# Kernel tuning notes

Measured on AMD Instinct MI355X. Metric: run time of the kernel, lower is better.

## Reference

```python
import jax, jax.numpy as jnp
import numpy as np

N_NODES = 100000


def setup_inputs() -> dict:
    key = jax.random.key(0)
    k1, k2, k3, k4, k5, k6 = jax.random.split(key, 6)
    x = jax.random.normal(k1, (N_NODES, 256), dtype=jnp.float32)
    edge_index = jax.random.randint(k2, (2, 3200000), 0, N_NODES, dtype=jnp.int64)
    # GCNConv(256, 3): glorot weight + zero bias (PyG default)
    lim1 = float(np.sqrt(6.0 / (256 + 3)))
    W1 = jax.random.uniform(k3, (256, 3), minval=-lim1, maxval=lim1, dtype=jnp.float32)
    b1 = jnp.zeros((3,), dtype=jnp.float32)
    # Linear(3, 7): torch default kaiming-uniform-ish bounds
    lim2 = float(1.0 / np.sqrt(3))
    W2 = jax.random.uniform(k4, (3, 7), minval=-lim2, maxval=lim2, dtype=jnp.float32)
    b2 = jax.random.uniform(k5, (7,), minval=-lim2, maxval=lim2, dtype=jnp.float32)
    return {"x": x, "edge_index": edge_index, "W1": W1, "b1": b1, "W2": W2, "b2": b2}


def gcn_conv(x, edge_index, W, b, num_nodes):
    # PyG GCNConv: add self-loops, symmetric deg^-1/2 (A+I) deg^-1/2 normalization,
    # aggregate transformed features, then add bias.
    loop = jnp.arange(num_nodes, dtype=edge_index.dtype)
    src = jnp.concatenate([edge_index[0], loop])
    dst = jnp.concatenate([edge_index[1], loop])
    ones = jnp.ones_like(dst, dtype=x.dtype)
    deg = jax.ops.segment_sum(ones, dst, num_segments=num_nodes)  # [N]
    dinv = jnp.where(deg > 0, jax.lax.rsqrt(deg), 0.0)
    norm = dinv[src] * dinv[dst]  # [E+N]
    h = x @ W  # [N, 3] — transform BEFORE gather (small width)
    msg = h[src] * norm[:, None]  # [E+N, 3]
    agg = jax.ops.segment_sum(msg, dst, num_segments=num_nodes)  # [N, 3]
    return agg + b


def reference(x, edge_index, W1, b1, W2, b2):
    h = jax.nn.relu(gcn_conv(x, edge_index, W1, b1, x.shape[0]))  # [N, 3]
    z = h @ W2 + b2  # [N, 7]
    return (h, z)
```

## Files before the change

kernel.cpp:

```cpp
#include <hip/hip_runtime.h>
#include <stdint.h>


#define BSHIFT 8
#define BNODES 256
#define OVFCAP 8192
#define STRIDE 64
#define PSTRIDE 192

__device__ __forceinline__ bool ei_is64(const unsigned* __restrict__ ei) {
    const int t = threadIdx.x;
    const int nz = (t < 256) && (ei[2 * t + 1] != 0u);
    return __syncthreads_or(nz) == 0;
}

__global__ __launch_bounds__(512) void k_pre(const float* __restrict__ x,
                                             const float* __restrict__ W1,
                                             float* __restrict__ g4,
                                             const unsigned* __restrict__ ei,
                                             unsigned* __restrict__ records,
                                             unsigned* __restrict__ pcnt,
                                             unsigned* __restrict__ ovf_cnt,
                                             unsigned* __restrict__ ovf,
                                             int E, int B, int CAP, int CH,
                                             int nbin, int N) {
    const bool is64 = ei_is64(ei);
    if ((int)blockIdx.x < nbin) {
        __shared__ unsigned cursor[512];
        for (int i = threadIdx.x; i < B; i += 512) cursor[i] = 0u;
        __syncthreads();
        const int e0 = blockIdx.x * CH;
        const int e1 = min(E, e0 + CH);
        const unsigned sbase = blockIdx.x * STRIDE;

        auto emit = [&](unsigned s, unsigned d) {
            const unsigned bb  = d >> BSHIFT;
            const unsigned idx = atomicAdd(&cursor[bb], 1u);
            if (idx < STRIDE) {
                records[(size_t)bb * CAP + sbase + idx] = (s << BSHIFT) | (d & (BNODES - 1));
            } else {
                const unsigned o = atomicAdd(ovf_cnt, 1u);
                if (o < OVFCAP) { ovf[2 * o] = s; ovf[2 * o + 1] = d; }
            }
        };

        const int nq = (e1 - e0) >> 2;
        if (is64) {
            const unsigned long long* e64 = (const unsigned long long*)ei;
            const ulonglong2* sp = (const ulonglong2*)(e64 + e0);
            const ulonglong2* dp = (const ulonglong2*)(e64 + (size_t)E + e0);
            for (int q = threadIdx.x; q < nq; q += 512) {
                const ulonglong2 sa = sp[2 * q], sb = sp[2 * q + 1];
                const ulonglong2 da = dp[2 * q], db = dp[2 * q + 1];
                emit((unsigned)sa.x, (unsigned)da.x);
                emit((unsigned)sa.y, (unsigned)da.y);
                emit((unsigned)sb.x, (unsigned)db.x);
                emit((unsigned)sb.y, (unsigned)db.y);
            }
            for (int e = e0 + 4 * nq + threadIdx.x; e < e1; e += 512)
                emit((unsigned)e64[e], (unsigned)e64[(size_t)E + e]);
        } else {
            const uint4* sp = (const uint4*)(ei + e0);
            const uint4* dp = (const uint4*)(ei + (size_t)E + e0);
            for (int q = threadIdx.x; q < nq; q += 512) {
                const uint4 s4 = sp[q], d4 = dp[q];
                emit(s4.x, d4.x);
                emit(s4.y, d4.y);
                emit(s4.z, d4.z);
                emit(s4.w, d4.w);
            }
            for (int e = e0 + 4 * nq + threadIdx.x; e < e1; e += 512)
                emit(ei[e], ei[(size_t)E + e]);
        }
        __syncthreads();
        for (int i = threadIdx.x; i < B; i += 512)
            pcnt[(size_t)i * PSTRIDE + blockIdx.x] = min(cursor[i], (unsigned)STRIDE);
    } else {
        const int bx      = blockIdx.x - nbin;
        const int gtid    = bx * 512 + threadIdx.x;
        const int nthread = ((int)gridDim.x - nbin) * 512;
        const int lane    = threadIdx.x & 63;
        float w[4][3];
#pragma unroll
        for (int k = 0; k < 4; ++k)
#pragma unroll
            for (int c = 0; c < 3; ++c)
                w[k][c] = W1[(lane * 4 + k) * 3 + c];
        const int wave   = gtid >> 6;
        const int nwaves = nthread >> 6;
        for (int node = wave; node < N; node += nwaves) {
            const float4 v = *reinterpret_cast<const float4*>(x + (size_t)node * 256 + lane * 4);
            float s0 = v.x * w[0][0] + v.y * w[1][0] + v.z * w[2][0] + v.w * w[3][0];
            float s1 = v.x * w[0][1] + v.y * w[1][1] + v.z * w[2][1] + v.w * w[3][1];
            float s2 = v.x * w[0][2] + v.y * w[1][2] + v.z * w[2][2] + v.w * w[3][2];
#pragma unroll
            for (int off = 32; off > 0; off >>= 1) {
                s0 += __shfl_xor(s0, off, 64);
                s1 += __shfl_xor(s1, off, 64);
                s2 += __shfl_xor(s2, off, 64);
            }
            if (lane == 0)
                reinterpret_cast<float4*>(g4)[node] = make_float4(s0, s1, s2, 0.f);
        }
    }
}

__global__ __launch_bounds__(256) void k_cnt2(const unsigned* __restrict__ records,
                                              const unsigned* __restrict__ pcnt,
                                              const unsigned* __restrict__ ovf_cnt,
                                              const unsigned* __restrict__ ovf,
                                              unsigned* __restrict__ pcount,
                                              int B, int CAP, int SPLIT, int nbin) {
    __shared__ unsigned cnt[BNODES];
    __shared__ unsigned scnt[PSTRIDE];
    const int b  = blockIdx.x / SPLIT;
    const int sl = blockIdx.x - b * SPLIT;
    cnt[threadIdx.x] = 0u;
    for (int i = threadIdx.x; i < nbin; i += 256) scnt[i] = pcnt[(size_t)b * PSTRIDE + i];
    __syncthreads();
    const int per = CAP / SPLIT;
    const int lo = sl * per, hi = lo + per;
    const unsigned* rec = records + (size_t)b * CAP;
    for (int k = lo + threadIdx.x; k < hi; k += 256) {
        if ((unsigned)(k & (STRIDE - 1)) < scnt[k >> 6])
            atomicAdd(&cnt[rec[k] & (BNODES - 1)], 1u);
    }
    if (sl == 0) {
        unsigned no = *ovf_cnt; if (no > OVFCAP) no = OVFCAP;
        for (unsigned i = threadIdx.x; i < no; i += 256) {
            const unsigned d = ovf[2 * i + 1];
            if ((int)(d >> BSHIFT) == b) atomicAdd(&cnt[d & (BNODES - 1)], 1u);
        }
    }
    __syncthreads();
    pcount[((size_t)blockIdx.x << BSHIFT) + threadIdx.x] = cnt[threadIdx.x];
}

__global__ __launch_bounds__(256) void k_dinv2(const unsigned* __restrict__ pcount,
                                               float* __restrict__ g4, int N, int SPLIT) {
    const int i = blockIdx.x * 256 + threadIdx.x;
    if (i >= N) return;
    const int b = i >> BSHIFT, t = i & (BNODES - 1);
    unsigned deg = 1u;
    for (int s = 0; s < SPLIT; ++s)
        deg += pcount[(((size_t)b * SPLIT + s) << BSHIFT) + t];
    const float r = rsqrtf((float)deg);
    const float4 h = reinterpret_cast<const float4*>(g4)[i];
    reinterpret_cast<float4*>(g4)[i] = make_float4(h.x * r, h.y * r, h.z * r, r);
}

__global__ __launch_bounds__(256) void k_msg2(const unsigned* __restrict__ records,
                                              const unsigned* __restrict__ pcnt,
                                              const unsigned* __restrict__ ovf_cnt,
                                              const unsigned* __restrict__ ovf,
                                              const float* __restrict__ g4,
                                              float* __restrict__ psum,
                                              int B, int CAP, int SPLIT, int nbin) {
    __shared__ float acc[BNODES * 3];
    __shared__ unsigned scnt[PSTRIDE];
    const int b  = blockIdx.x / SPLIT;
    const int sl = blockIdx.x - b * SPLIT;
    for (int i = threadIdx.x; i < BNODES * 3; i += 256) acc[i] = 0.f;
    for (int i = threadIdx.x; i < nbin; i += 256) scnt[i] = pcnt[(size_t)b * PSTRIDE + i];
    __syncthreads();
    const int per = CAP / SPLIT;
    const int lo = sl * per, hi = lo + per;
    const unsigned* rec = records + (size_t)b * CAP;
    const float4* g4v = reinterpret_cast<const float4*>(g4);
    for (int k = lo + threadIdx.x; k < hi; k += 256) {
        if ((unsigned)(k & (STRIDE - 1)) < scnt[k >> 6]) {
            const unsigned r = rec[k];
            const float4 g = g4v[r >> BSHIFT];
            const unsigned l = (r & (BNODES - 1)) * 3;
            atomicAdd(&acc[l + 0], g.x);
            atomicAdd(&acc[l + 1], g.y);
            atomicAdd(&acc[l + 2], g.z);
        }
    }
    if (sl == 0) {
        unsigned no = *ovf_cnt; if (no > OVFCAP) no = OVFCAP;
        for (unsigned i = threadIdx.x; i < no; i += 256) {
            const unsigned d = ovf[2 * i + 1];
            if ((int)(d >> BSHIFT) == b) {
                const float4 g = g4v[ovf[2 * i]];
                const unsigned l = (d & (BNODES - 1)) * 3;
                atomicAdd(&acc[l + 0], g.x);
                atomicAdd(&acc[l + 1], g.y);
                atomicAdd(&acc[l + 2], g.z);
            }
        }
    }
    __syncthreads();
    const size_t base = ((size_t)blockIdx.x * 3) << BSHIFT;
    psum[base +   0 + threadIdx.x] = acc[threadIdx.x * 3 + 0];
    psum[base + 256 + threadIdx.x] = acc[threadIdx.x * 3 + 1];
    psum[base + 512 + threadIdx.x] = acc[threadIdx.x * 3 + 2];
}

__global__ __launch_bounds__(256) void k_fin(const float* __restrict__ psum,
                                             const float* __restrict__ g4,
                                             const float* __restrict__ b1,
                                             const float* __restrict__ W2,
                                             const float* __restrict__ b2,
                                             float* __restrict__ out, int N, int SPLIT) {
    const int i = blockIdx.x * 256 + threadIdx.x;
    if (i >= N) return;
    const int b = i >> BSHIFT, t = i & (BNODES - 1);
    float a0 = 0.f, a1 = 0.f, a2 = 0.f;
    for (int s = 0; s < SPLIT; ++s) {
        const size_t base = (((size_t)b * SPLIT + s) * 3) << BSHIFT;
        a0 += psum[base + t];
        a1 += psum[base + 256 + t];
        a2 += psum[base + 512 + t];
    }
    const float4 g = reinterpret_cast<const float4*>(g4)[i];
    const float  r = g.w;
    const float h0 = fmaxf(r * (a0 + g.x) + b1[0], 0.f);
    const float h1 = fmaxf(r * (a1 + g.y) + b1[1], 0.f);
    const float h2 = fmaxf(r * (a2 + g.z) + b1[2], 0.f);
    out[3 * (size_t)i + 0] = h0;
    out[3 * (size_t)i + 1] = h1;
    out[3 * (size_t)i + 2] = h2;
    float* z = out + (size_t)3 * N;
#pragma unroll
    for (int c = 0; c < 7; ++c)
        z[7 * (size_t)i + c] = h0 * W2[c] + h1 * W2[7 + c] + h2 * W2[14 + c] + b2[c];
}

__global__ __launch_bounds__(256) void k_xw1_fb(const float* __restrict__ x,
                                                const float* __restrict__ W1,
                                                float* __restrict__ g4,
                                                unsigned* __restrict__ zptr,
                                                int nzero, int N) {
    const int gtid = blockIdx.x * 256 + threadIdx.x;
    const int nthread = gridDim.x * 256;
    for (int i = gtid; i < nzero; i += nthread) zptr[i] = 0u;
    const int lane = threadIdx.x & 63;
    float w[4][3];
#pragma unroll
    for (int k = 0; k < 4; ++k)
#pragma unroll
        for (int c = 0; c < 3; ++c) w[k][c] = W1[(lane * 4 + k) * 3 + c];
    const int wave = gtid >> 6, nwaves = nthread >> 6;
    for (int node = wave; node < N; node += nwaves) {
        const float4 v = *reinterpret_cast<const float4*>(x + (size_t)node * 256 + lane * 4);
        float s0 = v.x * w[0][0] + v.y * w[1][0] + v.z * w[2][0] + v.w * w[3][0];
        float s1 = v.x * w[0][1] + v.y * w[1][1] + v.z * w[2][1] + v.w * w[3][1];
        float s2 = v.x * w[0][2] + v.y * w[1][2] + v.z * w[2][2] + v.w * w[3][2];
#pragma unroll
        for (int off = 32; off > 0; off >>= 1) {
            s0 += __shfl_xor(s0, off, 64);
            s1 += __shfl_xor(s1, off, 64);
            s2 += __shfl_xor(s2, off, 64);
        }
        if (lane == 0)
            reinterpret_cast<float4*>(g4)[node] = make_float4(s0, s1, s2, 0.f);
    }
}
__global__ __launch_bounds__(256) void k_deg_fb(const unsigned* __restrict__ ei,
                                                float* __restrict__ deg, int E) {
    const bool is64 = ei_is64(ei);
    const int e = blockIdx.x * 256 + threadIdx.x;
    if (e >= E) return;
    const unsigned d = is64 ? (unsigned)((const unsigned long long*)ei)[(size_t)E + e]
                            : ei[(size_t)E + e];
    atomicAdd(&deg[d], 1.0f);
}
__global__ __launch_bounds__(256) void k_dinv_fb(const float* __restrict__ deg,
                                                 float* __restrict__ g4, int N) {
    const int i = blockIdx.x * 256 + threadIdx.x;
    if (i >= N) return;
    const float r = rsqrtf(1.0f + deg[i]);
    const float4 h = reinterpret_cast<const float4*>(g4)[i];
    reinterpret_cast<float4*>(g4)[i] = make_float4(h.x * r, h.y * r, h.z * r, r);
}
__global__ __launch_bounds__(256) void k_edge_fb(const unsigned* __restrict__ ei,
                                                 const float* __restrict__ g4,
                                                 float* __restrict__ u4, int E) {
    const bool is64 = ei_is64(ei);
    const int e = blockIdx.x * 256 + threadIdx.x;
    if (e >= E) return;
    unsigned s, d;
    if (is64) {
        const unsigned long long* q = (const unsigned long long*)ei;
        s = (unsigned)q[e]; d = (unsigned)q[(size_t)E + e];
    } else {
        s = ei[e]; d = ei[(size_t)E + e];
    }
    const float4 g = reinterpret_cast<const float4*>(g4)[s];
    atomicAdd(&u4[4 * (size_t)d + 0], g.x);
    atomicAdd(&u4[4 * (size_t)d + 1], g.y);
    atomicAdd(&u4[4 * (size_t)d + 2], g.z);
}
__global__ __launch_bounds__(256) void k_final_fb(const float* __restrict__ u4,
                                                  const float* __restrict__ g4,
                                                  const float* __restrict__ b1,
                                                  const float* __restrict__ W2,
                                                  const float* __restrict__ b2,
                                                  float* __restrict__ out, int N) {
    const int i = blockIdx.x * 256 + threadIdx.x;
    if (i >= N) return;
    const float4 g = reinterpret_cast<const float4*>(g4)[i];
    const float4 u = reinterpret_cast<const float4*>(u4)[i];
    const float  r = g.w;
    const float h0 = fmaxf(r * (u.x + g.x) + b1[0], 0.f);
    const float h1 = fmaxf(r * (u.y + g.y) + b1[1], 0.f);
    const float h2 = fmaxf(r * (u.z + g.z) + b1[2], 0.f);
    out[3 * (size_t)i + 0] = h0;
    out[3 * (size_t)i + 1] = h1;
    out[3 * (size_t)i + 2] = h2;
    float* z = out + (size_t)3 * N;
#pragma unroll
    for (int c = 0; c < 7; ++c)
        z[7 * (size_t)i + c] = h0 * W2[c] + h1 * W2[7 + c] + h2 * W2[14 + c] + b2[c];
}

extern "C" void kernel_launch(void* const* d_in, const int* in_sizes, int n_in,
                              void* d_out, int out_size, void* d_ws, size_t ws_size,
                              hipStream_t stream) {
    const float*    x   = (const float*)d_in[0];
    const unsigned* ei  = (const unsigned*)d_in[1];
    const float*    W1  = (const float*)d_in[2];
    const float*    b1  = (const float*)d_in[3];
    const float*    W2  = (const float*)d_in[4];
    const float*    b2  = (const float*)d_in[5];
    float*          out = (float*)d_out;

    const int N = in_sizes[0] / 256;
    const int E = in_sizes[1] / 2;
    const int B = (N + BNODES - 1) >> BSHIFT;

    int CH   = ((E + 189) / 190 + 3) & ~3;
    int nbin = (E + CH - 1) / CH;
    int CAP  = nbin * STRIDE;

    char*     ws      = (char*)d_ws;
    unsigned* ovf_cnt = (unsigned*)ws;
    size_t off = 256;
    float*    g4  = (float*)(ws + off);
    off = (off + 16ull * N + 255) & ~(size_t)255;
    unsigned* ovf = (unsigned*)(ws + off);
    off = (off + 8ull * OVFCAP + 255) & ~(size_t)255;
    unsigned* pcnt = (unsigned*)(ws + off);
    off = (off + 4ull * B * PSTRIDE + 255) & ~(size_t)255;
    const size_t puoff = off;

    int SPLIT = 0;
    size_t rec_off = 0;
    const int sps[4] = {8, 4, 2, 1};
    for (int si = 0; si < 4; ++si) {
        const int sp = sps[si];
        const size_t ro = (puoff + 4ull * B * sp * 768 + 255) & ~(size_t)255;
        if (ws_size >= ro + 4ull * B * CAP + 4096) { SPLIT = sp; rec_off = ro; break; }
    }

    if (SPLIT) {
        unsigned* pcount  = (unsigned*)(ws + puoff);
        float*    psum    = (float*)(ws + puoff);
        unsigned* records = (unsigned*)(ws + rec_off);
        hipMemsetAsync(ovf_cnt, 0, 4, stream);
        const int NBX = 2048;
        k_pre<<<nbin + NBX, 512, 0, stream>>>(x, W1, g4, ei, records, pcnt,
                                              ovf_cnt, ovf, E, B, CAP, CH, nbin, N);
        k_cnt2<<<B * SPLIT, 256, 0, stream>>>(records, pcnt, ovf_cnt, ovf, pcount,
                                              B, CAP, SPLIT, nbin);
        k_dinv2<<<(N + 255) / 256, 256, 0, stream>>>(pcount, g4, N, SPLIT);
        k_msg2<<<B * SPLIT, 256, 0, stream>>>(records, pcnt, ovf_cnt, ovf, g4, psum,
                                              B, CAP, SPLIT, nbin);
        k_fin<<<(N + 255) / 256, 256, 0, stream>>>(psum, g4, b1, W2, b2, out, N, SPLIT);
    } else {
        float* deg = (float*)(ws + puoff);
        float* u4  = deg + N;
        k_xw1_fb<<<4096, 256, 0, stream>>>(x, W1, g4, (unsigned*)deg, 5 * N, N);
        k_deg_fb<<<(E + 255) / 256, 256, 0, stream>>>(ei, deg, E);
        k_dinv_fb<<<(N + 255) / 256, 256, 0, stream>>>(deg, g4, N);
        k_edge_fb<<<(E + 255) / 256, 256, 0, stream>>>(ei, g4, u4, E);
        k_final_fb<<<(N + 255) / 256, 256, 0, stream>>>(u4, g4, b1, W2, b2, out, N);
    }
}
```

Before: 116.5 us.

## Use finer edge-binning geometry, higher split, and 4-nodes-per-wave GEMV

```diff
diff --git a/kernel.cpp b/kernel.cpp
--- a/kernel.cpp
+++ b/kernel.cpp
@@ -5,8 +5,7 @@
 #define BSHIFT 8
 #define BNODES 256
 #define OVFCAP 8192
-#define STRIDE 64
-#define PSTRIDE 192
+#define PSTRIDE 1024
 
 __device__ __forceinline__ bool ei_is64(const unsigned* __restrict__ ei) {
     const int t = threadIdx.x;
@@ -14,6 +13,7 @@
     return __syncthreads_or(nz) == 0;
 }
 
+template <int SSH>
 __global__ __launch_bounds__(512) void k_pre(const float* __restrict__ x,
                                              const float* __restrict__ W1,
                                              float* __restrict__ g4,
@@ -31,12 +31,12 @@
         __syncthreads();
         const int e0 = blockIdx.x * CH;
         const int e1 = min(E, e0 + CH);
-        const unsigned sbase = blockIdx.x * STRIDE;
+        const unsigned sbase = blockIdx.x << SSH;
 
         auto emit = [&](unsigned s, unsigned d) {
             const unsigned bb  = d >> BSHIFT;
             const unsigned idx = atomicAdd(&cursor[bb], 1u);
-            if (idx < STRIDE) {
+            if (idx < (1u << SSH)) {
                 records[(size_t)bb * CAP + sbase + idx] = (s << BSHIFT) | (d & (BNODES - 1));
             } else {
                 const unsigned o = atomicAdd(ovf_cnt, 1u);
@@ -74,37 +74,50 @@
         }
         __syncthreads();
         for (int i = threadIdx.x; i < B; i += 512)
-            pcnt[(size_t)i * PSTRIDE + blockIdx.x] = min(cursor[i], (unsigned)STRIDE);
+            pcnt[(size_t)i * PSTRIDE + blockIdx.x] = min(cursor[i], 1u << SSH);
     } else {
         const int bx      = blockIdx.x - nbin;
         const int gtid    = bx * 512 + threadIdx.x;
         const int nthread = ((int)gridDim.x - nbin) * 512;
         const int lane    = threadIdx.x & 63;
-        float w[4][3];
-#pragma unroll
-        for (int k = 0; k < 4; ++k)
-#pragma unroll
-            for (int c = 0; c < 3; ++c)
-                w[k][c] = W1[(lane * 4 + k) * 3 + c];
+        const int fg      = lane & 15;
+        const int m       = lane >> 4;
+        float w[4][4][3];
+#pragma unroll
+        for (int p = 0; p < 4; ++p)
+#pragma unroll
+            for (int j = 0; j < 4; ++j)
+#pragma unroll
+                for (int c = 0; c < 3; ++c)
+                    w[p][j][c] = W1[(fg * 4 + p * 64 + j) * 3 + c];
         const int wave   = gtid >> 6;
         const int nwaves = nthread >> 6;
-        for (int node = wave; node < N; node += nwaves) {
-            const float4 v = *reinterpret_cast<const float4*>(x + (size_t)node * 256 + lane * 4);
-            float s0 = v.x * w[0][0] + v.y * w[1][0] + v.z * w[2][0] + v.w * w[3][0];
-            float s1 = v.x * w[0][1] + v.y * w[1][1] + v.z * w[2][1] + v.w * w[3][1];
-            float s2 = v.x * w[0][2] + v.y * w[1][2] + v.z * w[2][2] + v.w * w[3][2];
-#pragma unroll
-            for (int off = 32; off > 0; off >>= 1) {
+        for (int nb4 = wave * 4; nb4 < N; nb4 += nwaves * 4) {
+            const int node = nb4 + m;
+            float s0 = 0.f, s1 = 0.f, s2 = 0.f;
+            if (node < N) {
+                const float* row = x + (size_t)node * 256 + fg * 4;
+#pragma unroll
+                for (int p = 0; p < 4; ++p) {
+                    const float4 v = *reinterpret_cast<const float4*>(row + p * 64);
+                    s0 += v.x * w[p][0][0] + v.y * w[p][1][0] + v.z * w[p][2][0] + v.w * w[p][3][0];
+                    s1 += v.x * w[p][0][1] + v.y * w[p][1][1] + v.z * w[p][2][1] + v.w * w[p][3][1];
+                    s2 += v.x * w[p][0][2] + v.y * w[p][1][2] + v.z * w[p][2][2] + v.w * w[p][3][2];
+                }
+            }
+#pragma unroll
+            for (int off = 8; off >= 1; off >>= 1) {
                 s0 += __shfl_xor(s0, off, 64);
                 s1 += __shfl_xor(s1, off, 64);
                 s2 += __shfl_xor(s2, off, 64);
             }
-            if (lane == 0)
+            if (fg == 0 && node < N)
                 reinterpret_cast<float4*>(g4)[node] = make_float4(s0, s1, s2, 0.f);
         }
     }
 }
 
+template <int SSH>
 __global__ __launch_bounds__(256) void k_cnt2(const unsigned* __restrict__ records,
                                               const unsigned* __restrict__ pcnt,
                                               const unsigned* __restrict__ ovf_cnt,
@@ -122,7 +135,7 @@
     const int lo = sl * per, hi = lo + per;
     const unsigned* rec = records + (size_t)b * CAP;
     for (int k = lo + threadIdx.x; k < hi; k += 256) {
-        if ((unsigned)(k & (STRIDE - 1)) < scnt[k >> 6])
+        if ((unsigned)(k & ((1 << SSH) - 1)) < scnt[k >> SSH])
             atomicAdd(&cnt[rec[k] & (BNODES - 1)], 1u);
     }
     if (sl == 0) {
@@ -149,6 +162,7 @@
     reinterpret_cast<float4*>(g4)[i] = make_float4(h.x * r, h.y * r, h.z * r, r);
 }
 
+template <int SSH>
 __global__ __launch_bounds__(256) void k_msg2(const unsigned* __restrict__ records,
                                               const unsigned* __restrict__ pcnt,
                                               const unsigned* __restrict__ ovf_cnt,
@@ -168,7 +182,7 @@
     const unsigned* rec = records + (size_t)b * CAP;
     const float4* g4v = reinterpret_cast<const float4*>(g4);
     for (int k = lo + threadIdx.x; k < hi; k += 256) {
-        if ((unsigned)(k & (STRIDE - 1)) < scnt[k >> 6]) {
+        if ((unsigned)(k & ((1 << SSH) - 1)) < scnt[k >> SSH]) {
             const unsigned r = rec[k];
             const float4 g = g4v[r >> BSHIFT];
             const unsigned l = (r & (BNODES - 1)) * 3;
@@ -330,9 +344,12 @@
     const int E = in_sizes[1] / 2;
     const int B = (N + BNODES - 1) >> BSHIFT;
 
-    int CH   = ((E + 189) / 190 + 3) & ~3;
-    int nbin = (E + CH - 1) / CH;
-    int CAP  = nbin * STRIDE;
+    const int CH_A   = ((E + 1019) / 1020 + 3) & ~3;
+    const int nbin_A = (E + CH_A - 1) / CH_A;
+    const int CAP_A  = nbin_A << 4;
+    const int CH_B   = ((E + 189) / 190 + 3) & ~3;
+    const int nbin_B = (E + CH_B - 1) / CH_B;
+    const int CAP_B  = nbin_B << 6;
 
     char*     ws      = (char*)d_ws;
     unsigned* ovf_cnt = (unsigned*)ws;
@@ -345,29 +362,55 @@
     off = (off + 4ull * B * PSTRIDE + 255) & ~(size_t)255;
     const size_t puoff = off;
 
-    int SPLIT = 0;
-    size_t rec_off = 0;
-    const int sps[4] = {8, 4, 2, 1};
-    for (int si = 0; si < 4; ++si) {
-        const int sp = sps[si];
-        const size_t ro = (puoff + 4ull * B * sp * 768 + 255) & ~(size_t)255;
-        if (ws_size >= ro + 4ull * B * CAP + 4096) { SPLIT = sp; rec_off = ro; break; }
-    }
-
-    if (SPLIT) {
+    struct Cfg { int ssh, nbin, cap, ch, split; size_t rec_off; };
+    Cfg cfg{0, 0, 0, 0, 0, 0};
+    const int geo_ssh[2]  = {4, 6};
+    const int geo_nbin[2] = {nbin_A, nbin_B};
+    const int geo_cap[2]  = {CAP_A, CAP_B};
+    const int geo_ch[2]   = {CH_A, CH_B};
+    const int sps[3]      = {16, 8, 4};
+    for (int gi = 0; gi < 2 && !cfg.split; ++gi) {
+        for (int si = 0; si < 3 && !cfg.split; ++si) {
+            const int sp = sps[si];
+            const size_t ro = (puoff + 4ull * B * sp * 768 + 255) & ~(size_t)255;
+            if (ws_size >= ro + 4ull * B * geo_cap[gi] + 4096) {
+                cfg.ssh = geo_ssh[gi]; cfg.nbin = geo_nbin[gi]; cfg.cap = geo_cap[gi];
+                cfg.ch = geo_ch[gi]; cfg.split = sp; cfg.rec_off = ro;
+            }
+        }
+    }
+
+    if (cfg.split) {
         unsigned* pcount  = (unsigned*)(ws + puoff);
         float*    psum    = (float*)(ws + puoff);
-        unsigned* records = (unsigned*)(ws + rec_off);
+        unsigned* records = (unsigned*)(ws + cfg.rec_off);
         hipMemsetAsync(ovf_cnt, 0, 4, stream);
-        const int NBX = 2048;
-        k_pre<<<nbin + NBX, 512, 0, stream>>>(x, W1, g4, ei, records, pcnt,
-                                              ovf_cnt, ovf, E, B, CAP, CH, nbin, N);
-        k_cnt2<<<B * SPLIT, 256, 0, stream>>>(records, pcnt, ovf_cnt, ovf, pcount,
-                                              B, CAP, SPLIT, nbin);
-        k_dinv2<<<(N + 255) / 256, 256, 0, stream>>>(pcount, g4, N, SPLIT);
-        k_msg2<<<B * SPLIT, 256, 0, stream>>>(records, pcnt, ovf_cnt, ovf, g4, psum,
-                                              B, CAP, SPLIT, nbin);
-        k_fin<<<(N + 255) / 256, 256, 0, stream>>>(psum, g4, b1, W2, b2, out, N, SPLIT);
+        const int NBX = 1024;
+        if (cfg.ssh == 4) {
+            k_pre<4><<<cfg.nbin + NBX, 512, 0, stream>>>(x, W1, g4, ei, records, pcnt,
+                                                         ovf_cnt, ovf, E, B, cfg.cap,
+                                                         cfg.ch, cfg.nbin, N);
+            k_cnt2<4><<<B * cfg.split, 256, 0, stream>>>(records, pcnt, ovf_cnt, ovf,
+                                                         pcount, B, cfg.cap, cfg.split,
+                                                         cfg.nbin);
+        } else {
+            k_pre<6><<<cfg.nbin + NBX, 512, 0, stream>>>(x, W1, g4, ei, records, pcnt,
+                                                         ovf_cnt, ovf, E, B, cfg.cap,
+                                                         cfg.ch, cfg.nbin, N);
+            k_cnt2<6><<<B * cfg.split, 256, 0, stream>>>(records, pcnt, ovf_cnt, ovf,
+                                                         pcount, B, cfg.cap, cfg.split,
+                                                         cfg.nbin);
+        }
+        k_dinv2<<<(N + 255) / 256, 256, 0, stream>>>(pcount, g4, N, cfg.split);
+        if (cfg.ssh == 4)
+            k_msg2<4><<<B * cfg.split, 256, 0, stream>>>(records, pcnt, ovf_cnt, ovf, g4,
+                                                         psum, B, cfg.cap, cfg.split,
+                                                         cfg.nbin);
+        else
+            k_msg2<6><<<B * cfg.split, 256, 0, stream>>>(records, pcnt, ovf_cnt, ovf, g4,
+                                                         psum, B, cfg.cap, cfg.split,
+                                                         cfg.nbin);
+        k_fin<<<(N + 255) / 256, 256, 0, stream>>>(psum, g4, b1, W2, b2, out, N, cfg.split);
     } else {
         float* deg = (float*)(ws + puoff);
         float* u4  = deg + N;
```

New measurement: 150.3 us. 29.0% more time.

## Split X·W1 and edge binning into separate kernels with finer strips

Applied to the files above, without the earlier changes.

```diff
diff --git a/kernel.cpp b/kernel.cpp
--- a/kernel.cpp
+++ b/kernel.cpp
@@ -4,9 +4,10 @@
 
 #define BSHIFT 8
 #define BNODES 256
-#define OVFCAP 8192
-#define STRIDE 64
-#define PSTRIDE 192
+#define OVFCAP 16384
+#define PSTRIDE 1024
+#define SSH 4
+#define SPLITC 4
 
 __device__ __forceinline__ bool ei_is64(const unsigned* __restrict__ ei) {
     const int t = threadIdx.x;
@@ -14,116 +15,138 @@
     return __syncthreads_or(nz) == 0;
 }
 
-__global__ __launch_bounds__(512) void k_pre(const float* __restrict__ x,
+__global__ __launch_bounds__(512) void k_xw1(const float* __restrict__ x,
                                              const float* __restrict__ W1,
-                                             float* __restrict__ g4,
-                                             const unsigned* __restrict__ ei,
-                                             unsigned* __restrict__ records,
-                                             unsigned* __restrict__ pcnt,
-                                             unsigned* __restrict__ ovf_cnt,
-                                             unsigned* __restrict__ ovf,
-                                             int E, int B, int CAP, int CH,
-                                             int nbin, int N) {
-    const bool is64 = ei_is64(ei);
-    if ((int)blockIdx.x < nbin) {
-        __shared__ unsigned cursor[512];
-        for (int i = threadIdx.x; i < B; i += 512) cursor[i] = 0u;
-        __syncthreads();
-        const int e0 = blockIdx.x * CH;
-        const int e1 = min(E, e0 + CH);
-        const unsigned sbase = blockIdx.x * STRIDE;
-
-        auto emit = [&](unsigned s, unsigned d) {
-            const unsigned bb  = d >> BSHIFT;
-            const unsigned idx = atomicAdd(&cursor[bb], 1u);
-            if (idx < STRIDE) {
-                records[(size_t)bb * CAP + sbase + idx] = (s << BSHIFT) | (d & (BNODES - 1));
-            } else {
-                const unsigned o = atomicAdd(ovf_cnt, 1u);
-                if (o < OVFCAP) { ovf[2 * o] = s; ovf[2 * o + 1] = d; }
-            }
-        };
-
-        const int nq = (e1 - e0) >> 2;
-        if (is64) {
-            const unsigned long long* e64 = (const unsigned long long*)ei;
-            const ulonglong2* sp = (const ulonglong2*)(e64 + e0);
-            const ulonglong2* dp = (const ulonglong2*)(e64 + (size_t)E + e0);
-            for (int q = threadIdx.x; q < nq; q += 512) {
-                const ulonglong2 sa = sp[2 * q], sb = sp[2 * q + 1];
-                const ulonglong2 da = dp[2 * q], db = dp[2 * q + 1];
-                emit((unsigned)sa.x, (unsigned)da.x);
-                emit((unsigned)sa.y, (unsigned)da.y);
-                emit((unsigned)sb.x, (unsigned)db.x);
-                emit((unsigned)sb.y, (unsigned)db.y);
-            }
-            for (int e = e0 + 4 * nq + threadIdx.x; e < e1; e += 512)
-                emit((unsigned)e64[e], (unsigned)e64[(size_t)E + e]);
-        } else {
-            const uint4* sp = (const uint4*)(ei + e0);
-            const uint4* dp = (const uint4*)(ei + (size_t)E + e0);
-            for (int q = threadIdx.x; q < nq; q += 512) {
-                const uint4 s4 = sp[q], d4 = dp[q];
-                emit(s4.x, d4.x);
-                emit(s4.y, d4.y);
-                emit(s4.z, d4.z);
-                emit(s4.w, d4.w);
-            }
-            for (int e = e0 + 4 * nq + threadIdx.x; e < e1; e += 512)
-                emit(ei[e], ei[(size_t)E + e]);
-        }
-        __syncthreads();
-        for (int i = threadIdx.x; i < B; i += 512)
-            pcnt[(size_t)i * PSTRIDE + blockIdx.x] = min(cursor[i], (unsigned)STRIDE);
-    } else {
-        const int bx      = blockIdx.x - nbin;
-        const int gtid    = bx * 512 + threadIdx.x;
-        const int nthread = ((int)gridDim.x - nbin) * 512;
-        const int lane    = threadIdx.x & 63;
-        float w[4][3];
-#pragma unroll
-        for (int k = 0; k < 4; ++k)
-#pragma unroll
-            for (int c = 0; c < 3; ++c)
-                w[k][c] = W1[(lane * 4 + k) * 3 + c];
-        const int wave   = gtid >> 6;
-        const int nwaves = nthread >> 6;
-        for (int node = wave; node < N; node += nwaves) {
-            const float4 v = *reinterpret_cast<const float4*>(x + (size_t)node * 256 + lane * 4);
-            float s0 = v.x * w[0][0] + v.y * w[1][0] + v.z * w[2][0] + v.w * w[3][0];
-            float s1 = v.x * w[0][1] + v.y * w[1][1] + v.z * w[2][1] + v.w * w[3][1];
-            float s2 = v.x * w[0][2] + v.y * w[1][2] + v.z * w[2][2] + v.w * w[3][2];
-#pragma unroll
-            for (int off = 32; off > 0; off >>= 1) {
+                                             float4* __restrict__ part4, int N) {
+    const int gtid   = blockIdx.x * 512 + threadIdx.x;
+    const int wave   = gtid >> 6;
+    const int nwaves = (gridDim.x * 512) >> 6;
+    const int lane   = threadIdx.x & 63;
+    const int fg     = lane & 15;
+    const int m      = lane >> 4;
+    const int f      = wave & 3;
+    const int wq     = wave >> 2;
+    const int wstep  = nwaves >> 2;
+
+    float w[4][3];
+#pragma unroll
+    for (int j = 0; j < 4; ++j)
+#pragma unroll
+        for (int c = 0; c < 3; ++c)
+            w[j][c] = W1[(f * 64 + fg * 4 + j) * 3 + c];
+
+    const int nq = (N + 3) >> 2;
+    for (int q = wq; q < nq; q += 4 * wstep) {
+        int nd[4]; bool ok[4]; float4 v[4];
+#pragma unroll
+        for (int u = 0; u < 4; ++u) {
+            const int qu = q + u * wstep;
+            nd[u] = qu * 4 + m;
+            ok[u] = (qu < nq) && (nd[u] < N);
+            v[u]  = ok[u] ? *reinterpret_cast<const float4*>(
+                                x + (size_t)nd[u] * 256 + f * 64 + fg * 4)
+                          : make_float4(0.f, 0.f, 0.f, 0.f);
+        }
+#pragma unroll
+        for (int u = 0; u < 4; ++u) {
+            float s0 = v[u].x * w[0][0] + v[u].y * w[1][0] + v[u].z * w[2][0] + v[u].w * w[3][0];
+            float s1 = v[u].x * w[0][1] + v[u].y * w[1][1] + v[u].z * w[2][1] + v[u].w * w[3][1];
+            float s2 = v[u].x * w[0][2] + v[u].y * w[1][2] + v[u].z * w[2][2] + v[u].w * w[3][2];
+#pragma unroll
+            for (int off = 8; off >= 1; off >>= 1) {
                 s0 += __shfl_xor(s0, off, 64);
                 s1 += __shfl_xor(s1, off, 64);
                 s2 += __shfl_xor(s2, off, 64);
             }
-            if (lane == 0)
-                reinterpret_cast<float4*>(g4)[node] = make_float4(s0, s1, s2, 0.f);
-        }
-    }
-}
-
-__global__ __launch_bounds__(256) void k_cnt2(const unsigned* __restrict__ records,
+            if (ok[u] && fg == 0)
+                part4[(size_t)f * N + nd[u]] = make_float4(s0, s1, s2, 0.f);
+        }
+    }
+}
+
+__global__ __launch_bounds__(512) void k_bin(const unsigned* __restrict__ ei,
+                                             unsigned* __restrict__ records,
+                                             uint8_t* __restrict__ low8,
+                                             unsigned* __restrict__ pcnt,
+                                             unsigned* __restrict__ ovf_cnt,
+                                             unsigned* __restrict__ ovf,
+                                             int E, int B, int CAP, int CH) {
+    const bool is64 = ei_is64(ei);
+    __shared__ unsigned cursor[512];
+    for (int i = threadIdx.x; i < B; i += 512) cursor[i] = 0u;
+    __syncthreads();
+    const int e0 = blockIdx.x * CH;
+    const int e1 = min(E, e0 + CH);
+    const unsigned sbase = blockIdx.x << SSH;
+
+    auto emit = [&](unsigned s, unsigned d) {
+        const unsigned bb  = d >> BSHIFT;
+        const unsigned idx = atomicAdd(&cursor[bb], 1u);
+        if (idx < (1u << SSH)) {
+            const size_t slot = (size_t)bb * CAP + sbase + idx;
+            records[slot] = (s << BSHIFT) | (d & (BNODES - 1));
+            low8[slot]    = (uint8_t)(d & (BNODES - 1));
+        } else {
+            const unsigned o = atomicAdd(ovf_cnt, 1u);
+            if (o < OVFCAP) { ovf[2 * o] = s; ovf[2 * o + 1] = d; }
+        }
+    };
+
+    const int nq = (e1 - e0) >> 2;
+    if (is64) {
+        const unsigned long long* e64 = (const unsigned long long*)ei;
+        const ulonglong2* sp = (const ulonglong2*)(e64 + e0);
+        const ulonglong2* dp = (const ulonglong2*)(e64 + (size_t)E + e0);
+        for (int q = threadIdx.x; q < nq; q += 512) {
+            const ulonglong2 sa = sp[2 * q], sb = sp[2 * q + 1];
+            const ulonglong2 da = dp[2 * q], db = dp[2 * q + 1];
+            emit((unsigned)sa.x, (unsigned)da.x);
+            emit((unsigned)sa.y, (unsigned)da.y);
+            emit((unsigned)sb.x, (unsigned)db.x);
+            emit((unsigned)sb.y, (unsigned)db.y);
+        }
+        for (int e = e0 + 4 * nq + threadIdx.x; e < e1; e += 512)
+            emit((unsigned)e64[e], (unsigned)e64[(size_t)E + e]);
+    } else {
+        const uint4* sp = (const uint4*)(ei + e0);
+        const uint4* dp = (const uint4*)(ei + (size_t)E + e0);
+        for (int q = threadIdx.x; q < nq; q += 512) {
+            const uint4 s4 = sp[q], d4 = dp[q];
+            emit(s4.x, d4.x);
+            emit(s4.y, d4.y);
+            emit(s4.z, d4.z);
+            emit(s4.w, d4.w);
+        }
+        for (int e = e0 + 4 * nq + threadIdx.x; e < e1; e += 512)
+            emit(ei[e], ei[(size_t)E + e]);
+    }
+    __syncthreads();
+    for (int i = threadIdx.x; i < B; i += 512)
+        pcnt[(size_t)i * PSTRIDE + blockIdx.x] = min(cursor[i], 1u << SSH);
+}
+
+__global__ __launch_bounds__(256) void k_cnt2(const uint8_t* __restrict__ low8,
                                               const unsigned* __restrict__ pcnt,
                                               const unsigned* __restrict__ ovf_cnt,
                                               const unsigned* __restrict__ ovf,
                                               unsigned* __restrict__ pcount,
-                                              int B, int CAP, int SPLIT, int nbin) {
+                                              int B, int CAP, int nbin) {
     __shared__ unsigned cnt[BNODES];
-    __shared__ unsigned scnt[PSTRIDE];
-    const int b  = blockIdx.x / SPLIT;
-    const int sl = blockIdx.x - b * SPLIT;
+    const int b  = blockIdx.x / SPLITC;
+    const int sl = blockIdx.x - b * SPLITC;
     cnt[threadIdx.x] = 0u;
-    for (int i = threadIdx.x; i < nbin; i += 256) scnt[i] = pcnt[(size_t)b * PSTRIDE + i];
-    __syncthreads();
-    const int per = CAP / SPLIT;
-    const int lo = sl * per, hi = lo + per;
-    const unsigned* rec = records + (size_t)b * CAP;
-    for (int k = lo + threadIdx.x; k < hi; k += 256) {
-        if ((unsigned)(k & (STRIDE - 1)) < scnt[k >> 6])
-            atomicAdd(&cnt[rec[k] & (BNODES - 1)], 1u);
+    __syncthreads();
+    const int strip = sl * 256 + threadIdx.x;
+    if (strip < nbin) {
+        const unsigned c = pcnt[(size_t)b * PSTRIDE + strip];
+        const uint4 lv = *reinterpret_cast<const uint4*>(
+            low8 + (size_t)b * CAP + ((size_t)strip << SSH));
+#define CNT_BYTE(word, sh, idx) if ((idx) < c) atomicAdd(&cnt[((word) >> (sh)) & 255u], 1u);
+        CNT_BYTE(lv.x,  0, 0u) CNT_BYTE(lv.x,  8, 1u) CNT_BYTE(lv.x, 16, 2u) CNT_BYTE(lv.x, 24, 3u)
+        CNT_BYTE(lv.y,  0, 4u) CNT_BYTE(lv.y,  8, 5u) CNT_BYTE(lv.y, 16, 6u) CNT_BYTE(lv.y, 24, 7u)
+        CNT_BYTE(lv.z,  0, 8u) CNT_BYTE(lv.z,  8, 9u) CNT_BYTE(lv.z, 16, 10u) CNT_BYTE(lv.z, 24, 11u)
+        CNT_BYTE(lv.w,  0, 12u) CNT_BYTE(lv.w,  8, 13u) CNT_BYTE(lv.w, 16, 14u) CNT_BYTE(lv.w, 24, 15u)
+#undef CNT_BYTE
     }
     if (sl == 0) {
         unsigned no = *ovf_cnt; if (no > OVFCAP) no = OVFCAP;
@@ -136,17 +159,25 @@
     pcount[((size_t)blockIdx.x << BSHIFT) + threadIdx.x] = cnt[threadIdx.x];
 }
 
-__global__ __launch_bounds__(256) void k_dinv2(const unsigned* __restrict__ pcount,
-                                               float* __restrict__ g4, int N, int SPLIT) {
+__global__ __launch_bounds__(256) void k_dinv2(const float4* __restrict__ part4,
+                                               const unsigned* __restrict__ pcount,
+                                               float* __restrict__ g4, int N) {
     const int i = blockIdx.x * 256 + threadIdx.x;
     if (i >= N) return;
     const int b = i >> BSHIFT, t = i & (BNODES - 1);
+    const float4 p0 = part4[i];
+    const float4 p1 = part4[(size_t)N + i];
+    const float4 p2 = part4[(size_t)2 * N + i];
+    const float4 p3 = part4[(size_t)3 * N + i];
+    const float hx = p0.x + p1.x + p2.x + p3.x;
+    const float hy = p0.y + p1.y + p2.y + p3.y;
+    const float hz = p0.z + p1.z + p2.z + p3.z;
     unsigned deg = 1u;
-    for (int s = 0; s < SPLIT; ++s)
-        deg += pcount[(((size_t)b * SPLIT + s) << BSHIFT) + t];
+#pragma unroll
+    for (int s = 0; s < SPLITC; ++s)
+        deg += pcount[(((size_t)b * SPLITC + s) << BSHIFT) + t];
     const float r = rsqrtf((float)deg);
-    const float4 h = reinterpret_cast<const float4*>(g4)[i];
-    reinterpret_cast<float4*>(g4)[i] = make_float4(h.x * r, h.y * r, h.z * r, r);
+    reinterpret_cast<float4*>(g4)[i] = make_float4(hx * r, hy * r, hz * r, r);
 }
 
 __global__ __launch_bounds__(256) void k_msg2(const unsigned* __restrict__ records,
@@ -155,27 +186,33 @@
                                               const unsigned* __restrict__ ovf,
                                               const float* __restrict__ g4,
                                               float* __restrict__ psum,
-                                              int B, int CAP, int SPLIT, int nbin) {
+                                              int B, int CAP, int nbin) {
     __shared__ float acc[BNODES * 3];
-    __shared__ unsigned scnt[PSTRIDE];
-    const int b  = blockIdx.x / SPLIT;
-    const int sl = blockIdx.x - b * SPLIT;
+    const int b  = blockIdx.x / SPLITC;
+    const int sl = blockIdx.x - b * SPLITC;
     for (int i = threadIdx.x; i < BNODES * 3; i += 256) acc[i] = 0.f;
-    for (int i = threadIdx.x; i < nbin; i += 256) scnt[i] = pcnt[(size_t)b * PSTRIDE + i];
-    __syncthreads();
-    const int per = CAP / SPLIT;
-    const int lo = sl * per, hi = lo + per;
-    const unsigned* rec = records + (size_t)b * CAP;
+    __syncthreads();
     const float4* g4v = reinterpret_cast<const float4*>(g4);
-    for (int k = lo + threadIdx.x; k < hi; k += 256) {
-        if ((unsigned)(k & (STRIDE - 1)) < scnt[k >> 6]) {
-            const unsigned r = rec[k];
-            const float4 g = g4v[r >> BSHIFT];
-            const unsigned l = (r & (BNODES - 1)) * 3;
-            atomicAdd(&acc[l + 0], g.x);
-            atomicAdd(&acc[l + 1], g.y);
-            atomicAdd(&acc[l + 2], g.z);
-        }
+    const int strip = sl * 256 + threadIdx.x;
+    if (strip < nbin) {
+        const unsigned c = pcnt[(size_t)b * PSTRIDE + strip];
+        const uint4* rp = reinterpret_cast<const uint4*>(
+            records + (size_t)b * CAP + ((size_t)strip << SSH));
+        const uint4 r0 = rp[0], r1 = rp[1], r2 = rp[2], r3 = rp[3];
+#define MSG_REC(word, idx)                                         \
+        if ((idx) < c) {                                           \
+            const unsigned rr = (word);                            \
+            const float4 g = g4v[rr >> BSHIFT];                    \
+            const unsigned l = (rr & (BNODES - 1)) * 3;            \
+            atomicAdd(&acc[l + 0], g.x);                           \
+            atomicAdd(&acc[l + 1], g.y);                           \
+            atomicAdd(&acc[l + 2], g.z);                           \
+        }
+        MSG_REC(r0.x, 0u) MSG_REC(r0.y, 1u) MSG_REC(r0.z, 2u) MSG_REC(r0.w, 3u)
+        MSG_REC(r1.x, 4u) MSG_REC(r1.y, 5u) MSG_REC(r1.z, 6u) MSG_REC(r1.w, 7u)
+        MSG_REC(r2.x, 8u) MSG_REC(r2.y, 9u) MSG_REC(r2.z, 10u) MSG_REC(r2.w, 11u)
+        MSG_REC(r3.x, 12u) MSG_REC(r3.y, 13u) MSG_REC(r3.z, 14u) MSG_REC(r3.w, 15u)
+#undef MSG_REC
     }
     if (sl == 0) {
         unsigned no = *ovf_cnt; if (no > OVFCAP) no = OVFCAP;
@@ -202,13 +239,14 @@
                                              const float* __restrict__ b1,
                                              const float* __restrict__ W2,
                                              const float* __restrict__ b2,
-                                             float* __restrict__ out, int N, int SPLIT) {
+                                             float* __restrict__ out, int N) {
     const int i = blockIdx.x * 256 + threadIdx.x;
     if (i >= N) return;
     const int b = i >> BSHIFT, t = i & (BNODES - 1);
     float a0 = 0.f, a1 = 0.f, a2 = 0.f;
-    for (int s = 0; s < SPLIT; ++s) {
-        const size_t base = (((size_t)b * SPLIT + s) * 3) << BSHIFT;
+#pragma unroll
+    for (int s = 0; s < SPLITC; ++s) {
+        const size_t base = (((size_t)b * SPLITC + s) * 3) << BSHIFT;
         a0 += psum[base + t];
         a1 += psum[base + 256 + t];
         a2 += psum[base + 512 + t];
@@ -330,46 +368,39 @@
     const int E = in_sizes[1] / 2;
     const int B = (N + BNODES - 1) >> BSHIFT;
 
-    int CH   = ((E + 189) / 190 + 3) & ~3;
-    int nbin = (E + CH - 1) / CH;
-    int CAP  = nbin * STRIDE;
+    const int CH   = ((E + 1019) / 1020 + 3) & ~3;
+    const int nbin = (E + CH - 1) / CH;
+    const int CAP  = nbin << SSH;
 
     char*     ws      = (char*)d_ws;
     unsigned* ovf_cnt = (unsigned*)ws;
     size_t off = 256;
-    float*    g4  = (float*)(ws + off);
+    float*    g4    = (float*)(ws + off);
     off = (off + 16ull * N + 255) & ~(size_t)255;
-    unsigned* ovf = (unsigned*)(ws + off);
+    float4*   part4 = (float4*)(ws + off);
+    off = (off + 64ull * N + 255) & ~(size_t)255;
+    unsigned* ovf   = (unsigned*)(ws + off);
     off = (off + 8ull * OVFCAP + 255) & ~(size_t)255;
-    unsigned* pcnt = (unsigned*)(ws + off);
+    unsigned* pcnt  = (unsigned*)(ws + off);
     off = (off + 4ull * B * PSTRIDE + 255) & ~(size_t)255;
-    const size_t puoff = off;
-
-    int SPLIT = 0;
-    size_t rec_off = 0;
-    const int sps[4] = {8, 4, 2, 1};
-    for (int si = 0; si < 4; ++si) {
-        const int sp = sps[si];
-        const size_t ro = (puoff + 4ull * B * sp * 768 + 255) & ~(size_t)255;
-        if (ws_size >= ro + 4ull * B * CAP + 4096) { SPLIT = sp; rec_off = ro; break; }
-    }
-
-    if (SPLIT) {
-        unsigned* pcount  = (unsigned*)(ws + puoff);
-        float*    psum    = (float*)(ws + puoff);
-        unsigned* records = (unsigned*)(ws + rec_off);
+    unsigned* pcount = (unsigned*)(ws + off);
+    float*    psum   = (float*)(ws + off);
+    off = (off + 4ull * B * SPLITC * 768 + 255) & ~(size_t)255;
+    uint8_t*  low8   = (uint8_t*)(ws + off);
+    off = (off + (size_t)B * CAP + 255) & ~(size_t)255;
+    unsigned* records = (unsigned*)(ws + off);
+    const size_t need = off + 4ull * B * CAP + 4096;
+
+    if (ws_size >= need) {
         hipMemsetAsync(ovf_cnt, 0, 4, stream);
-        const int NBX = 2048;
-        k_pre<<<nbin + NBX, 512, 0, stream>>>(x, W1, g4, ei, records, pcnt,
-                                              ovf_cnt, ovf, E, B, CAP, CH, nbin, N);
-        k_cnt2<<<B * SPLIT, 256, 0, stream>>>(records, pcnt, ovf_cnt, ovf, pcount,
-                                              B, CAP, SPLIT, nbin);
-        k_dinv2<<<(N + 255) / 256, 256, 0, stream>>>(pcount, g4, N, SPLIT);
-        k_msg2<<<B * SPLIT, 256, 0, stream>>>(records, pcnt, ovf_cnt, ovf, g4, psum,
-                                              B, CAP, SPLIT, nbin);
-        k_fin<<<(N + 255) / 256, 256, 0, stream>>>(psum, g4, b1, W2, b2, out, N, SPLIT);
+        k_xw1<<<1024, 512, 0, stream>>>(x, W1, part4, N);
+        k_bin<<<nbin, 512, 0, stream>>>(ei, records, low8, pcnt, ovf_cnt, ovf, E, B, CAP, CH);
+        k_cnt2<<<B * SPLITC, 256, 0, stream>>>(low8, pcnt, ovf_cnt, ovf, pcount, B, CAP, nbin);
+        k_dinv2<<<(N + 255) / 256, 256, 0, stream>>>(part4, pcount, g4, N);
+        k_msg2<<<B * SPLITC, 256, 0, stream>>>(records, pcnt, ovf_cnt, ovf, g4, psum, B, CAP, nbin);
+        k_fin<<<(N + 255) / 256, 256, 0, stream>>>(psum, g4, b1, W2, b2, out, N);
     } else {
-        float* deg = (float*)(ws + puoff);
+        float* deg = (float*)part4;
         float* u4  = deg + N;
         k_xw1_fb<<<4096, 256, 0, stream>>>(x, W1, g4, (unsigned*)deg, 5 * N, N);
         k_deg_fb<<<(E + 255) / 256, 256, 0, stream>>>(ei, deg, E);
```

New measurement: 176.9 us. 1.52x slower.
